# Kernel tuning notes

Hardware: AMD Instinct MI355X
Metric: run time of the kernel (lower is better)

Reference implementation:

```python
import jax, jax.numpy as jnp
import numpy as np

IN_FEATURES = 64
WIDTH = 64
GRID_POINTS = 64   # num control points / basis functions
DEGREE = 3
BATCH = 32768
LN_EPS = 1e-5


def make_knots():
    # clamped knot vector on [0, 1]: length = GRID_POINTS + DEGREE + 1
    knot_count = GRID_POINTS + DEGREE + 1
    knots = np.zeros(knot_count, dtype=np.float32)
    knots[-(DEGREE + 1):] = 1.0
    interior = knot_count - 2 * (DEGREE + 1)
    if interior > 0:
        knots[DEGREE + 1: DEGREE + 1 + interior] = np.linspace(0.0, 1.0, interior + 2, dtype=np.float32)[1:-1]
    return jnp.asarray(knots)


def bspline_basis(x, knots):
    # x: [B, F] in (0,1); vectorized Cox-de Boor across batch and features
    xx = x[..., None]                      # [B, F, 1]
    left, right = knots[:-1], knots[1:]
    b = ((xx >= left) & (xx < right)).astype(x.dtype)      # [B, F, n_basis]
    last = ((x >= left[-1]) & (x <= right[-1])).astype(x.dtype)
    b = jnp.concatenate([b[..., :-1], last[..., None]], axis=-1)
    n_basis = knots.shape[0] - 1
    for d in range(1, DEGREE + 1):
        upper = n_basis - d
        i = np.arange(upper)
        k_i, k_id = knots[i], knots[i + d]
        k_i1, k_id1 = knots[i + 1], knots[i + d + 1]
        den1, den2 = k_id - k_i, k_id1 - k_i1
        w1 = jnp.where(den1 > 0, (xx - k_i) / jnp.where(den1 > 0, den1, 1.0), 0.0)
        w2 = jnp.where(den2 > 0, (k_id1 - xx) / jnp.where(den2 > 0, den2, 1.0), 0.0)
        b = w1 * b[..., :upper] + w2 * b[..., 1:upper + 1]
    return b  # [B, F, GRID_POINTS]


def setup_inputs() -> dict:
    key = jax.random.key(0)
    ks = jax.random.split(key, 6)
    coeff_init = float(np.sqrt(2.0 / (GRID_POINTS * IN_FEATURES)))
    return {
        "inputs": jax.random.normal(ks[0], (BATCH, IN_FEATURES), dtype=jnp.float32),
        "input_shift": 0.1 * jax.random.normal(ks[1], (IN_FEATURES,), dtype=jnp.float32),
        "input_log_scale": 0.1 * jax.random.normal(ks[2], (IN_FEATURES,), dtype=jnp.float32),
        "spline_coeffs": coeff_init * jax.random.normal(ks[3], (IN_FEATURES, GRID_POINTS, WIDTH), dtype=jnp.float32),
        "skip_W": jax.random.normal(ks[4], (WIDTH, IN_FEATURES), dtype=jnp.float32) / np.sqrt(IN_FEATURES),
        "skip_b": 0.01 * jax.random.normal(ks[5], (WIDTH,), dtype=jnp.float32),
        "bias": jnp.zeros((WIDTH,), dtype=jnp.float32),
        "ln_gamma": jnp.ones((WIDTH,), dtype=jnp.float32),
        "ln_beta": jnp.zeros((WIDTH,), dtype=jnp.float32),
        "knots": make_knots(),
    }


def reference(inputs, input_shift, input_log_scale, spline_coeffs, skip_W, skip_b, bias, ln_gamma, ln_beta, knots):
    scale = jax.nn.softplus(input_log_scale) + 0.001
    normalised = jax.nn.sigmoid((inputs - input_shift) * scale)     # [B, F]
    basis = bspline_basis(normalised, knots)                        # [B, F, G]
    spline_mix = jnp.einsum('bfg,fgw->bw', basis, spline_coeffs)    # [B, W]
    skip = inputs @ skip_W.T + skip_b
    c = spline_mix + skip + bias
    mean = jnp.mean(c, axis=-1, keepdims=True)
    var = jnp.mean((c - mean) ** 2, axis=-1, keepdims=True)
    y = (c - mean) / jnp.sqrt(var + LN_EPS) * ln_gamma + ln_beta
    return jax.nn.gelu(y, approximate=False)
```

## Files before the change

### kernel.cpp

```cpp
#include <hip/hip_runtime.h>
#include <math.h>


#define NTHREADS 512
#define ROWSB 32
#define SLABF 16384

typedef float v2f  __attribute__((ext_vector_type(2)));
typedef short bf16x8 __attribute__((ext_vector_type(8)));
typedef float f32x4  __attribute__((ext_vector_type(4)));

#if __has_builtin(__builtin_amdgcn_sdot4)
#define SDOT4(a, b, c) __builtin_amdgcn_sdot4((int)(a), (int)(b), (c), false)
#else
__device__ __forceinline__ int sdot4_sw(unsigned a, unsigned b, int c) {
    return c + (int)(signed char)(a) * (int)(signed char)(b)
             + (int)(signed char)(a >> 8)  * (int)(signed char)(b >> 8)
             + (int)(signed char)(a >> 16) * (int)(signed char)(b >> 16)
             + (int)(signed char)(a >> 24) * (int)(signed char)(b >> 24);
}
#define SDOT4(a, b, c) sdot4_sw((a), (b), (c))
#endif

__device__ __forceinline__ unsigned int f2bf1(float f) {
    unsigned int u = __float_as_uint(f);
    return (u + 0x7fffu + ((u >> 16) & 1u)) >> 16;
}
__device__ __forceinline__ unsigned int q8(float v) {
    const float s = fminf(fmaxf(v * 512.f, -127.f), 127.f);
    return (unsigned int)((int)rintf(s)) & 255u;
}

__global__ __launch_bounds__(256) void kan_prep(
    const float* __restrict__ coeff_g,
    unsigned char* __restrict__ ws8)
{
    const int idx = blockIdx.x * 256 + threadIdx.x;
    const int f = idx / 3904;
    const int rem = idx - f * 3904;
    const int g0 = rem >> 6, w = rem & 63;
    const float* src = coeff_g + ((size_t)f << 12) + (g0 << 6) + w;
    const unsigned int d = q8(src[0])
                         | (q8(src[64])  << 8)
                         | (q8(src[128]) << 16)
                         | (q8(src[192]) << 24);
    *(unsigned int*)(ws8 + ((size_t)f << 14) + (g0 << 8) + (w << 2)) = d;
}

template<bool PRE>
__global__ __launch_bounds__(NTHREADS, 6) void kan_fused(
    const float* __restrict__ x_g,
    const float* __restrict__ shift_g,
    const float* __restrict__ lsc_g,
    const float* __restrict__ coeff_g,
    const float* __restrict__ skipW_g,
    const float* __restrict__ skipb_g,
    const float* __restrict__ bias_g,
    const float* __restrict__ gamma_g,
    const float* __restrict__ beta_g,
    const float* __restrict__ knots_g,
    const unsigned char* __restrict__ ws8,
    float* __restrict__ out_g)
{
    __shared__ float  xin[64][ROWSB];
    __shared__ unsigned short xb[32 * 64];
    __shared__ unsigned short wst[64 * 64];
    __shared__ float  skps[32][64];
    __shared__ uint2  wtab2[16 * 32];
    __shared__ float  knot_s[68];
    __shared__ float  scale_s[64];
    __shared__ float  shift_s[64];

    const int t = threadIdx.x;
    const int row0 = blockIdx.x * ROWSB;

    {
        const int r = t >> 4, f0 = (t & 15) << 2;
        const float4 a = *((const float4*)(x_g + (size_t)(row0 + r) * 64 + f0));
        xin[f0 + 0][r] = a.x; xin[f0 + 1][r] = a.y;
        xin[f0 + 2][r] = a.z; xin[f0 + 3][r] = a.w;
        uint2 p;
        p.x = f2bf1(a.x) | (f2bf1(a.y) << 16);
        p.y = f2bf1(a.z) | (f2bf1(a.w) << 16);
        const int byte = r * 128 + ((((t & 15) << 3)) ^ ((r & 7) << 4));
        *(uint2*)((char*)xb + byte) = p;
    }
    {
        const int w = t >> 3, f0 = (t & 7) << 3;
        const float4* src = (const float4*)(skipW_g + (size_t)w * 64 + f0);
        const float4 a0 = src[0], a1 = src[1];
        uint4 p;
        p.x = f2bf1(a0.x) | (f2bf1(a0.y) << 16);
        p.y = f2bf1(a0.z) | (f2bf1(a0.w) << 16);
        p.z = f2bf1(a1.x) | (f2bf1(a1.y) << 16);
        p.w = f2bf1(a1.z) | (f2bf1(a1.w) << 16);
        const int byte = w * 128 + ((((t & 7) << 4)) ^ ((w & 7) << 4));
        *(uint4*)((char*)wst + byte) = p;
    }
    if (t < 64) {
        scale_s[t] = log1pf(__expf(lsc_g[t])) + 0.001f;
        shift_s[t] = shift_g[t];
    }
    if (t < 68) knot_s[t] = knots_g[t];
    __syncthreads();

    const int lane = t & 63;
    const int wave = t >> 6;

    {
        const int mtile = wave >> 2;
        const int ntile = wave & 3;
        const int arow = mtile * 16 + (lane & 15);
        const int bcol = ntile * 16 + (lane & 15);
        const int koff = (lane >> 4) << 4;
        f32x4 acc = {0.f, 0.f, 0.f, 0.f};
        #pragma unroll
        for (int kb = 0; kb < 2; ++kb) {
            const int kbyte = (kb << 6) + koff;
            const bf16x8 af = *(const bf16x8*)((const char*)xb
                                + arow * 128 + (kbyte ^ ((arow & 7) << 4)));
            const bf16x8 bfr = *(const bf16x8*)((const char*)wst
                                + bcol * 128 + (kbyte ^ ((bcol & 7) << 4)));
            acc = __builtin_amdgcn_mfma_f32_16x16x32_bf16(af, bfr, acc, 0, 0, 0);
        }
        #pragma unroll
        for (int rr = 0; rr < 4; ++rr)
            skps[mtile * 16 + ((lane >> 4) << 2) + rr][bcol] = acc[rr];
    }

    const int wc   = lane & 15;
    const int rsub = lane >> 4;
    const int row  = (wave << 2) + rsub;
    const int w4   = wc << 2;

    int doti[4] = {0, 0, 0, 0};
    float facc[4] = {0.f, 0.f, 0.f, 0.f};
    const unsigned char* const wbase = ws8 + (wc << 4);

    for (int g = 0; g < 4; ++g) {
        __syncthreads();
        {
            const int fc_ = t >> 5, r_ = t & 31;
            const int feat = (g << 4) + fc_;
            const float xs = (xin[feat][r_] - shift_s[feat]) * scale_s[feat];
            const float xq = 1.f / (1.f + __expf(-xs));
            int m = (int)floorf(xq * 61.f);
            m = m < 0 ? 0 : (m > 60 ? 60 : m);
            const int i = m + 3;
            float left[4], right[4], N[4];
            N[0] = 1.f;
            #pragma unroll
            for (int j = 1; j <= 3; ++j) {
                left[j]  = xq - knot_s[i + 1 - j];
                right[j] = knot_s[i + j] - xq;
                float saved = 0.f;
                #pragma unroll
                for (int rr = 0; rr < j; ++rr) {
                    const float temp = N[rr] * __builtin_amdgcn_rcpf(right[rr + 1] + left[j - rr]);
                    N[rr] = saved + right[rr + 1] * temp;
                    saved = left[j - rr] * temp;
                }
                N[j] = saved;
            }
            const unsigned int q0 = (unsigned int)(int)(fmaxf(N[0], 0.f) * 126.f + 0.5f);
            const unsigned int q1 = (unsigned int)(int)(fmaxf(N[1], 0.f) * 126.f + 0.5f);
            const unsigned int q2 = (unsigned int)(int)(fmaxf(N[2], 0.f) * 126.f + 0.5f);
            const unsigned int q3 = (unsigned int)(int)(fmaxf(N[3], 0.f) * 126.f + 0.5f);
            wtab2[t] = make_uint2(q0 | (q1 << 8) | (q2 << 16) | (q3 << 24),
                                  (unsigned int)(m << 8));
        }
        __syncthreads();

        if (PRE) {
            const unsigned char* const gbase = wbase + ((size_t)g << 18);
            #pragma unroll
            for (int h = 0; h < 4; ++h) {
                const uint2 wv0 = wtab2[(((h << 2) + 0) << 5) + row];
                const uint2 wv1 = wtab2[(((h << 2) + 1) << 5) + row];
                const uint2 wv2 = wtab2[(((h << 2) + 2) << 5) + row];
                const uint2 wv3 = wtab2[(((h << 2) + 3) << 5) + row];
                const uint4 A0 = *((const uint4*)(gbase + (((h << 2) + 0) << 14) + wv0.y));
                const uint4 A1 = *((const uint4*)(gbase + (((h << 2) + 1) << 14) + wv1.y));
                const uint4 A2 = *((const uint4*)(gbase + (((h << 2) + 2) << 14) + wv2.y));
                const uint4 A3 = *((const uint4*)(gbase + (((h << 2) + 3) << 14) + wv3.y));
                doti[0] = SDOT4(wv0.x, A0.x, doti[0]);
                doti[1] = SDOT4(wv0.x, A0.y, doti[1]);
                doti[2] = SDOT4(wv0.x, A0.z, doti[2]);
                doti[3] = SDOT4(wv0.x, A0.w, doti[3]);
                doti[0] = SDOT4(wv1.x, A1.x, doti[0]);
                doti[1] = SDOT4(wv1.x, A1.y, doti[1]);
                doti[2] = SDOT4(wv1.x, A1.z, doti[2]);
                doti[3] = SDOT4(wv1.x, A1.w, doti[3]);
                doti[0] = SDOT4(wv2.x, A2.x, doti[0]);
                doti[1] = SDOT4(wv2.x, A2.y, doti[1]);
                doti[2] = SDOT4(wv2.x, A2.z, doti[2]);
                doti[3] = SDOT4(wv2.x, A2.w, doti[3]);
                doti[0] = SDOT4(wv3.x, A3.x, doti[0]);
                doti[1] = SDOT4(wv3.x, A3.y, doti[1]);
                doti[2] = SDOT4(wv3.x, A3.z, doti[2]);
                doti[3] = SDOT4(wv3.x, A3.w, doti[3]);
            }
        } else {
            #pragma unroll 2
            for (int fc = 0; fc < 16; ++fc) {
                const int f = (g << 4) + fc;
                const uint2 wv = wtab2[(fc << 5) + row];
                const float* cb = coeff_g + ((size_t)f << 12) + (wv.y >> 2) + w4;
                const float4 c0 = *((const float4*)cb);
                const float4 c1 = *((const float4*)(cb + 64));
                const float4 c2 = *((const float4*)(cb + 128));
                const float4 c3 = *((const float4*)(cb + 192));
                const float q0 = (float)(wv.x & 255u);
                const float q1 = (float)((wv.x >> 8) & 255u);
                const float q2 = (float)((wv.x >> 16) & 255u);
                const float q3 = (float)((wv.x >> 24) & 255u);
                facc[0] += q0 * c0.x + q1 * c1.x + q2 * c2.x + q3 * c3.x;
                facc[1] += q0 * c0.y + q1 * c1.y + q2 * c2.y + q3 * c3.y;
                facc[2] += q0 * c0.z + q1 * c1.z + q2 * c2.z + q3 * c3.z;
                facc[3] += q0 * c0.w + q1 * c1.w + q2 * c2.w + q3 * c3.w;
            }
        }
    }

    const float4 sk = *((const float4*)(&skps[row][w4]));
    const float4 sb = *((const float4*)(skipb_g + w4));
    const float4 bi = *((const float4*)(bias_g + w4));
    const float4 ga = *((const float4*)(gamma_g + w4));
    const float4 be = *((const float4*)(beta_g + w4));
    const float add_[4] = {sk.x + sb.x + bi.x, sk.y + sb.y + bi.y,
                           sk.z + sb.z + bi.z, sk.w + sb.w + bi.w};
    const float gam[4] = {ga.x, ga.y, ga.z, ga.w};
    const float bet[4] = {be.x, be.y, be.z, be.w};
    const float cs = PRE ? (1.f / (512.f * 126.f)) : (1.f / 126.f);

    float c[4];
    #pragma unroll
    for (int k = 0; k < 4; ++k) {
        const float sp = PRE ? (float)doti[k] * cs : facc[k] * cs;
        c[k] = sp + add_[k];
    }
    float s = c[0] + c[1] + c[2] + c[3];
    s += __shfl_xor(s, 1); s += __shfl_xor(s, 2);
    s += __shfl_xor(s, 4); s += __shfl_xor(s, 8);
    const float mean = s * 0.015625f;
    float v = 0.f;
    #pragma unroll
    for (int k = 0; k < 4; ++k) { const float d = c[k] - mean; v += d * d; }
    v += __shfl_xor(v, 1); v += __shfl_xor(v, 2);
    v += __shfl_xor(v, 4); v += __shfl_xor(v, 8);
    const float inv = rsqrtf(v * 0.015625f + 1e-5f);
    float o[4];
    #pragma unroll
    for (int k = 0; k < 4; ++k) {
        const float y = (c[k] - mean) * inv * gam[k] + bet[k];
        o[k] = 0.5f * y * (1.f + erff(y * 0.70710678118f));
    }
    *((float4*)(out_g + (size_t)(row0 + row) * 64 + w4)) =
        make_float4(o[0], o[1], o[2], o[3]);
}

extern "C" void kernel_launch(void* const* d_in, const int* in_sizes, int n_in,
                              void* d_out, int out_size, void* d_ws, size_t ws_size,
                              hipStream_t stream) {
    (void)in_sizes; (void)n_in; (void)out_size;
    const bool pre = (ws_size >= (size_t)(64 * SLABF));
    if (pre) {
        kan_prep<<<976, 256, 0, stream>>>((const float*)d_in[3], (unsigned char*)d_ws);
        kan_fused<true><<<1024, NTHREADS, 0, stream>>>(
            (const float*)d_in[0], (const float*)d_in[1], (const float*)d_in[2],
            (const float*)d_in[3], (const float*)d_in[4], (const float*)d_in[5],
            (const float*)d_in[6], (const float*)d_in[7], (const float*)d_in[8],
            (const float*)d_in[9], (const unsigned char*)d_ws, (float*)d_out);
    } else {
        kan_fused<false><<<1024, NTHREADS, 0, stream>>>(
            (const float*)d_in[0], (const float*)d_in[1], (const float*)d_in[2],
            (const float*)d_in[3], (const float*)d_in[4], (const float*)d_in[5],
            (const float*)d_in[6], (const float*)d_in[7], (const float*)d_in[8],
            (const float*)d_in[9], (const unsigned char*)d_ws, (float*)d_out);
    }
}
```

Measured before the change: 35.14 us.

## Double-buffer basis table and overlap next-group basis eval with dot loads

Replaces the per-group basis table with a double-buffered row-major table, so each feature group's basis weights are computed while the previous group's int8 coefficient gathers are in flight. One barrier per group is removed. Interior knot spans now use a closed-form uniform cubic B-spline instead of Cox-de Boor, and table reads become vectorized uint4 loads. The cost is more live registers and shared memory, which may lower occupancy, and the closed form could round slightly differently from the recursion.

```diff
diff --git a/kernel.cpp b/kernel.cpp
--- a/kernel.cpp
+++ b/kernel.cpp
@@ -6,7 +6,6 @@
 #define ROWSB 32
 #define SLABF 16384
 
-typedef float v2f  __attribute__((ext_vector_type(2)));
 typedef short bf16x8 __attribute__((ext_vector_type(8)));
 typedef float f32x4  __attribute__((ext_vector_type(4)));
 
@@ -46,6 +45,12 @@
                          | (q8(src[192]) << 24);
     *(unsigned int*)(ws8 + ((size_t)f << 14) + (g0 << 8) + (w << 2)) = d;
 }
+
+#define DOT4Q(WP, AV) do { \
+    doti[0] = SDOT4((WP), (AV).x, doti[0]); \
+    doti[1] = SDOT4((WP), (AV).y, doti[1]); \
+    doti[2] = SDOT4((WP), (AV).z, doti[2]); \
+    doti[3] = SDOT4((WP), (AV).w, doti[3]); } while (0)
 
 template<bool PRE>
 __global__ __launch_bounds__(NTHREADS, 6) void kan_fused(
@@ -66,13 +71,56 @@
     __shared__ unsigned short xb[32 * 64];
     __shared__ unsigned short wst[64 * 64];
     __shared__ float  skps[32][64];
-    __shared__ uint2  wtab2[16 * 32];
+    __shared__ uint2  wtabd[2][32][20];
     __shared__ float  knot_s[68];
     __shared__ float  scale_s[64];
     __shared__ float  shift_s[64];
 
     const int t = threadIdx.x;
     const int row0 = blockIdx.x * ROWSB;
+
+    auto basis_group = [&](int gb) {
+        const int fc_ = t >> 5, r_ = t & 31;
+        const int feat = (gb << 4) + fc_;
+        const float xs = (xin[feat][r_] - shift_s[feat]) * scale_s[feat];
+        const float xq = 1.f / (1.f + __expf(-xs));
+        int m = (int)floorf(xq * 61.f);
+        m = m < 0 ? 0 : (m > 60 ? 60 : m);
+        const float u = fmaf(xq, 61.f, -(float)m);
+        float N0, N1, N2, N3;
+        if (__builtin_expect(m >= 2 && m <= 58, 1)) {
+            const float omu = 1.f - u;
+            const float u2 = u * u, u3 = u2 * u;
+            N0 = omu * omu * omu * (1.f / 6.f);
+            N3 = u3 * (1.f / 6.f);
+            N1 = 0.5f * u3 - u2 + (2.f / 3.f);
+            N2 = 1.f - N0 - N1 - N3;
+        } else {
+            const int i = m + 3;
+            float left[4], right[4], N[4];
+            N[0] = 1.f;
+            #pragma unroll
+            for (int j = 1; j <= 3; ++j) {
+                left[j]  = xq - knot_s[i + 1 - j];
+                right[j] = knot_s[i + j] - xq;
+                float saved = 0.f;
+                #pragma unroll
+                for (int rr = 0; rr < j; ++rr) {
+                    const float temp = N[rr] * __builtin_amdgcn_rcpf(right[rr + 1] + left[j - rr]);
+                    N[rr] = saved + right[rr + 1] * temp;
+                    saved = left[j - rr] * temp;
+                }
+                N[j] = saved;
+            }
+            N0 = N[0]; N1 = N[1]; N2 = N[2]; N3 = N[3];
+        }
+        const unsigned int q0 = (unsigned int)(int)(fmaxf(N0, 0.f) * 126.f + 0.5f);
+        const unsigned int q1 = (unsigned int)(int)(fmaxf(N1, 0.f) * 126.f + 0.5f);
+        const unsigned int q2 = (unsigned int)(int)(fmaxf(N2, 0.f) * 126.f + 0.5f);
+        const unsigned int q3 = (unsigned int)(int)(fmaxf(N3, 0.f) * 126.f + 0.5f);
+        wtabd[gb & 1][r_][fc_] = make_uint2(q0 | (q1 << 8) | (q2 << 16) | (q3 << 24),
+                                            (unsigned int)(m << 8));
+    };
 
     {
         const int r = t >> 4, f0 = (t & 15) << 2;
@@ -132,79 +180,57 @@
     const int rsub = lane >> 4;
     const int row  = (wave << 2) + rsub;
     const int w4   = wc << 2;
+    const int wcb  = wc << 4;
 
     int doti[4] = {0, 0, 0, 0};
     float facc[4] = {0.f, 0.f, 0.f, 0.f};
-    const unsigned char* const wbase = ws8 + (wc << 4);
+
+    basis_group(0);
+    __syncthreads();
 
     for (int g = 0; g < 4; ++g) {
-        __syncthreads();
-        {
-            const int fc_ = t >> 5, r_ = t & 31;
-            const int feat = (g << 4) + fc_;
-            const float xs = (xin[feat][r_] - shift_s[feat]) * scale_s[feat];
-            const float xq = 1.f / (1.f + __expf(-xs));
-            int m = (int)floorf(xq * 61.f);
-            m = m < 0 ? 0 : (m > 60 ? 60 : m);
-            const int i = m + 3;
-            float left[4], right[4], N[4];
-            N[0] = 1.f;
-            #pragma unroll
-            for (int j = 1; j <= 3; ++j) {
-                left[j]  = xq - knot_s[i + 1 - j];
-                right[j] = knot_s[i + j] - xq;
-                float saved = 0.f;
-                #pragma unroll
-                for (int rr = 0; rr < j; ++rr) {
-                    const float temp = N[rr] * __builtin_amdgcn_rcpf(right[rr + 1] + left[j - rr]);
-                    N[rr] = saved + right[rr + 1] * temp;
-                    saved = left[j - rr] * temp;
-                }
-                N[j] = saved;
-            }
-            const unsigned int q0 = (unsigned int)(int)(fmaxf(N[0], 0.f) * 126.f + 0.5f);
-            const unsigned int q1 = (unsigned int)(int)(fmaxf(N[1], 0.f) * 126.f + 0.5f);
-            const unsigned int q2 = (unsigned int)(int)(fmaxf(N[2], 0.f) * 126.f + 0.5f);
-            const unsigned int q3 = (unsigned int)(int)(fmaxf(N[3], 0.f) * 126.f + 0.5f);
-            wtab2[t] = make_uint2(q0 | (q1 << 8) | (q2 << 16) | (q3 << 24),
-                                  (unsigned int)(m << 8));
-        }
-        __syncthreads();
-
+        const uint2* wrow = &wtabd[g & 1][row][0];
         if (PRE) {
-            const unsigned char* const gbase = wbase + ((size_t)g << 18);
-            #pragma unroll
-            for (int h = 0; h < 4; ++h) {
-                const uint2 wv0 = wtab2[(((h << 2) + 0) << 5) + row];
-                const uint2 wv1 = wtab2[(((h << 2) + 1) << 5) + row];
-                const uint2 wv2 = wtab2[(((h << 2) + 2) << 5) + row];
-                const uint2 wv3 = wtab2[(((h << 2) + 3) << 5) + row];
-                const uint4 A0 = *((const uint4*)(gbase + (((h << 2) + 0) << 14) + wv0.y));
-                const uint4 A1 = *((const uint4*)(gbase + (((h << 2) + 1) << 14) + wv1.y));
-                const uint4 A2 = *((const uint4*)(gbase + (((h << 2) + 2) << 14) + wv2.y));
-                const uint4 A3 = *((const uint4*)(gbase + (((h << 2) + 3) << 14) + wv3.y));
-                doti[0] = SDOT4(wv0.x, A0.x, doti[0]);
-                doti[1] = SDOT4(wv0.x, A0.y, doti[1]);
-                doti[2] = SDOT4(wv0.x, A0.z, doti[2]);
-                doti[3] = SDOT4(wv0.x, A0.w, doti[3]);
-                doti[0] = SDOT4(wv1.x, A1.x, doti[0]);
-                doti[1] = SDOT4(wv1.x, A1.y, doti[1]);
-                doti[2] = SDOT4(wv1.x, A1.z, doti[2]);
-                doti[3] = SDOT4(wv1.x, A1.w, doti[3]);
-                doti[0] = SDOT4(wv2.x, A2.x, doti[0]);
-                doti[1] = SDOT4(wv2.x, A2.y, doti[1]);
-                doti[2] = SDOT4(wv2.x, A2.z, doti[2]);
-                doti[3] = SDOT4(wv2.x, A2.w, doti[3]);
-                doti[0] = SDOT4(wv3.x, A3.x, doti[0]);
-                doti[1] = SDOT4(wv3.x, A3.y, doti[1]);
-                doti[2] = SDOT4(wv3.x, A3.z, doti[2]);
-                doti[3] = SDOT4(wv3.x, A3.w, doti[3]);
-            }
+            const unsigned char* const gbase = ws8 + ((size_t)g << 18);
+            const uint4 wpa = *(const uint4*)(wrow + 0);
+            const uint4 wpb = *(const uint4*)(wrow + 2);
+            const uint4 wpc = *(const uint4*)(wrow + 4);
+            const uint4 wpd = *(const uint4*)(wrow + 6);
+            const uint4 A0 = *(const uint4*)(gbase + (0 << 14) + (wpa.y | wcb));
+            const uint4 A1 = *(const uint4*)(gbase + (1 << 14) + (wpa.w | wcb));
+            const uint4 A2 = *(const uint4*)(gbase + (2 << 14) + (wpb.y | wcb));
+            const uint4 A3 = *(const uint4*)(gbase + (3 << 14) + (wpb.w | wcb));
+            const uint4 A4 = *(const uint4*)(gbase + (4 << 14) + (wpc.y | wcb));
+            const uint4 A5 = *(const uint4*)(gbase + (5 << 14) + (wpc.w | wcb));
+            const uint4 A6 = *(const uint4*)(gbase + (6 << 14) + (wpd.y | wcb));
+            const uint4 A7 = *(const uint4*)(gbase + (7 << 14) + (wpd.w | wcb));
+            if (g < 3) basis_group(g + 1);
+            DOT4Q(wpa.x, A0); DOT4Q(wpa.z, A1);
+            DOT4Q(wpb.x, A2); DOT4Q(wpb.z, A3);
+            DOT4Q(wpc.x, A4); DOT4Q(wpc.z, A5);
+            DOT4Q(wpd.x, A6); DOT4Q(wpd.z, A7);
+            const uint4 wpe = *(const uint4*)(wrow + 8);
+            const uint4 wpf = *(const uint4*)(wrow + 10);
+            const uint4 wpg = *(const uint4*)(wrow + 12);
+            const uint4 wph = *(const uint4*)(wrow + 14);
+            const uint4 B0 = *(const uint4*)(gbase + (8 << 14)  + (wpe.y | wcb));
+            const uint4 B1 = *(const uint4*)(gbase + (9 << 14)  + (wpe.w | wcb));
+            const uint4 B2 = *(const uint4*)(gbase + (10 << 14) + (wpf.y | wcb));
+            const uint4 B3 = *(const uint4*)(gbase + (11 << 14) + (wpf.w | wcb));
+            const uint4 B4 = *(const uint4*)(gbase + (12 << 14) + (wpg.y | wcb));
+            const uint4 B5 = *(const uint4*)(gbase + (13 << 14) + (wpg.w | wcb));
+            const uint4 B6 = *(const uint4*)(gbase + (14 << 14) + (wph.y | wcb));
+            const uint4 B7 = *(const uint4*)(gbase + (15 << 14) + (wph.w | wcb));
+            DOT4Q(wpe.x, B0); DOT4Q(wpe.z, B1);
+            DOT4Q(wpf.x, B2); DOT4Q(wpf.z, B3);
+            DOT4Q(wpg.x, B4); DOT4Q(wpg.z, B5);
+            DOT4Q(wph.x, B6); DOT4Q(wph.z, B7);
         } else {
+            if (g < 3) basis_group(g + 1);
             #pragma unroll 2
             for (int fc = 0; fc < 16; ++fc) {
                 const int f = (g << 4) + fc;
-                const uint2 wv = wtab2[(fc << 5) + row];
+                const uint2 wv = wrow[fc];
                 const float* cb = coeff_g + ((size_t)f << 12) + (wv.y >> 2) + w4;
                 const float4 c0 = *((const float4*)cb);
                 const float4 c1 = *((const float4*)(cb + 64));
@@ -220,6 +246,7 @@
                 facc[3] += q0 * c0.w + q1 * c1.w + q2 * c2.w + q3 * c3.w;
             }
         }
+        __syncthreads();
     }
 
     const float4 sk = *((const float4*)(&skps[row][w4]));
```

Measured after the change: 35.41 us. No clear change (+0.8%).
